# Optimization experiments

Hardware: AMD Instinct MI355X
Metric: run time of the kernel (lower is better)

Reference implementation:

```python
import jax, jax.numpy as jnp
import numpy as np

B, S, EMBED, HEADS = 2, 2048, 2048, 16
HEAD_DIM = EMBED // HEADS  # 128


def setup_inputs() -> dict:
    key = jax.random.key(0)
    k1, k2, k3 = jax.random.split(key, 3)
    x = jax.random.normal(k1, (B, S, EMBED), dtype=jnp.float32)
    # qkv_proj: Linear(EMBED -> 3*EMBED, bias=False); stored as [in, out]
    w_qkv = jax.random.normal(k2, (EMBED, 3 * EMBED), dtype=jnp.float32) / np.float32(np.sqrt(EMBED))
    # out_proj: Linear(EMBED -> EMBED, bias=False)
    w_out = jax.random.normal(k3, (EMBED, EMBED), dtype=jnp.float32) / np.float32(np.sqrt(EMBED))
    return {"x": x, "w_qkv": w_qkv, "w_out": w_out}


def reference(x, w_qkv, w_out):
    b, s, e = x.shape
    h, d = HEADS, e // HEADS
    qkv = x @ w_qkv                                  # [b, s, 3e]
    q, k, v = jnp.split(qkv, 3, axis=-1)             # each [b, s, e]
    q = q.reshape(b, s, h, d).transpose(0, 2, 1, 3)  # [b, h, s, d]
    k = k.reshape(b, s, h, d).transpose(0, 2, 1, 3)
    v = v.reshape(b, s, h, d).transpose(0, 2, 1, 3)
    scale = jnp.asarray(1.0 / np.sqrt(d), dtype=q.dtype)
    scores = jnp.einsum('bhqd,bhkd->bhqk', q, k) * scale  # [b, h, s, s]
    causal = jnp.tril(jnp.ones((s, s), dtype=bool))
    scores = jnp.where(causal, scores, -jnp.inf)
    attn = jax.nn.softmax(scores, axis=-1)
    ctx = jnp.einsum('bhqk,bhkd->bhqd', attn, v)     # [b, h, s, d]
    ctx = ctx.transpose(0, 2, 1, 3).reshape(b, s, e)
    return ctx @ w_out
```

## Files before the change

### kernel.cpp

```cpp
#include <hip/hip_runtime.h>
#include <cstdint>

#define S_LEN 2048
#define EMB   2048
#define NHEAD 16
#define HDIM  128
#define MROWS 4096
#define NQKV  6144

typedef __bf16 bf16x8 __attribute__((ext_vector_type(8)));
typedef __bf16 bf16x4 __attribute__((ext_vector_type(4)));
typedef float  f32x4  __attribute__((ext_vector_type(4)));

#define MFMA16(a, b, c) __builtin_amdgcn_mfma_f32_16x16x32_bf16((a), (b), (c), 0, 0, 0)

__device__ __forceinline__ unsigned short f2bf(float f) {
  unsigned u = __builtin_bit_cast(unsigned, f);
  u += 0x7fffu + ((u >> 16) & 1u);
  return (unsigned short)(u >> 16);
}
__device__ __forceinline__ float bf2f(unsigned short u) {
  unsigned v = ((unsigned)u) << 16;
  return __builtin_bit_cast(float, v);
}

__device__ __forceinline__ void gl_lds16(const unsigned short* g, unsigned short* l) {
  __builtin_amdgcn_global_load_lds(
      (const __attribute__((address_space(1))) void*)(uintptr_t)g,
      (__attribute__((address_space(3))) void*)(unsigned int)(uintptr_t)l,
      16, 0, 0);
}

__global__ void cast_bf16(const float* __restrict__ in, unsigned short* __restrict__ out, int n) {
  int i = (blockIdx.x * 256 + threadIdx.x) * 4;
  if (i >= n) return;
  float4 v = *(const float4*)(in + i);
  ushort4 o;
  o.x = f2bf(v.x); o.y = f2bf(v.y); o.z = f2bf(v.z); o.w = f2bf(v.w);
  *(ushort4*)(out + i) = o;
}

__global__ void transpose_cast(const float* __restrict__ in, unsigned short* __restrict__ out,
                               int R, int C) {
  __shared__ float tile[32][33];
  int bx = blockIdx.x << 5;
  int by = blockIdx.y << 5;
  int tx = threadIdx.x, ty = threadIdx.y;
  for (int j = 0; j < 32; j += 8)
    tile[ty + j][tx] = in[(size_t)(by + ty + j) * C + bx + tx];
  __syncthreads();
  for (int j = 0; j < 32; j += 8)
    out[(size_t)(bx + ty + j) * R + by + tx] = f2bf(tile[tx][ty + j]);
}

__global__ __launch_bounds__(256, 3) void gemm_qkv(const unsigned short* __restrict__ A,
                                                   const unsigned short* __restrict__ Bt,
                                                   unsigned short* __restrict__ Qo,
                                                   unsigned short* __restrict__ Ko,
                                                   unsigned short* __restrict__ Vt) {
  __shared__ __align__(16) unsigned short As[128 * 64];
  __shared__ __align__(16) unsigned short Bs[128 * 64];
  const int tid = threadIdx.x;
  const int n0 = blockIdx.x << 7;
  const int m0 = blockIdx.y << 7;
  const int wave = tid >> 6, lane = tid & 63;
  const int wm = (wave & 1) << 6, wn = (wave >> 1) << 6;
  const int fr = lane & 15, g = lane >> 4;
  const int q = tid >> 3;
  const int jp = tid & 7;
  f32x4 acc[4][4] = {};
  for (int k0 = 0; k0 < 2048; k0 += 64) {
    for (int i = 0; i < 4; ++i) {
      const int row = q + (i << 5);
      const int jsw = (jp ^ (row & 7)) << 3;
      gl_lds16(A + (size_t)(m0 + row) * 2048 + k0 + jsw, As + (row << 6) + (jp << 3));
      gl_lds16(Bt + (size_t)(n0 + row) * 2048 + k0 + jsw, Bs + (row << 6) + (jp << 3));
    }
    __builtin_amdgcn_s_waitcnt(0);
    __syncthreads();
    for (int ks = 0; ks < 2; ++ks) {
      const int slot = (((ks << 2) + g) ^ (fr & 7)) << 3;
      bf16x8 af[4], bfv[4];
      for (int i = 0; i < 4; ++i) af[i]  = *(const bf16x8*)(As + ((wm + (i << 4) + fr) << 6) + slot);
      for (int j = 0; j < 4; ++j) bfv[j] = *(const bf16x8*)(Bs + ((wn + (j << 4) + fr) << 6) + slot);
      for (int i = 0; i < 4; ++i)
        for (int j = 0; j < 4; ++j)
          acc[i][j] = MFMA16(af[i], bfv[j], acc[i][j]);
    }
    __syncthreads();
  }
  const int which = n0 >> 11;
  const int h = (n0 >> 7) & 15;
  const int bb = m0 >> 11;
  const int bh = bb * NHEAD + h;
  for (int i = 0; i < 4; ++i) {
    const int sl = (m0 & (S_LEN - 1)) + wm + (i << 4) + (g << 2);
    for (int j = 0; j < 4; ++j) {
      const int d = wn + (j << 4) + fr;
      if (which == 2) {
        ushort4 pk;
        pk.x = f2bf(acc[i][j][0]); pk.y = f2bf(acc[i][j][1]);
        pk.z = f2bf(acc[i][j][2]); pk.w = f2bf(acc[i][j][3]);
        *(ushort4*)(Vt + ((size_t)bh * HDIM + d) * S_LEN + sl) = pk;
      } else {
        unsigned short* dst = (which == 0) ? Qo : Ko;
        for (int r = 0; r < 4; ++r)
          dst[((size_t)bh * S_LEN + sl + r) * HDIM + d] = f2bf(acc[i][j][r]);
      }
    }
  }
}

__global__ __launch_bounds__(256, 3) void attn(const unsigned short* __restrict__ Qg,
                                               const unsigned short* __restrict__ Kg,
                                               const unsigned short* __restrict__ Vtg,
                                               unsigned short* __restrict__ ctx,
                                               unsigned short* __restrict__ Opart,
                                               float* __restrict__ Lp) {
  __shared__ __align__(16) unsigned short SA[16384];
  __shared__ __align__(16) unsigned short Ps[8192];
  unsigned short* Qs = SA;
  unsigned short* Ks = SA;
  unsigned short* Vs = SA + 8192;

  const int blk = blockIdx.x;
  const int bh = blk & 31;
  const int t = blk >> 5;
  int qt, kt0, nkt, part;
  if (t < 8)       { qt = t;     kt0 = 0;  nkt = 2 * t + 2;       part = -1; }
  else if (t < 16) { qt = t;     kt0 = 0;  nkt = 16;              part = (bh << 3) + (qt - 8); }
  else             { qt = t - 8; kt0 = 16; nkt = 2 * qt - 14;     part = 256 + (bh << 3) + (qt - 8); }

  const int tid = threadIdx.x, wave = tid >> 6, lane = tid & 63;
  const int fr = lane & 15, g = lane >> 4;

  const unsigned short* qsrc = Qg + ((size_t)bh * S_LEN + (qt << 7)) * HDIM;
  for (int i = 0; i < 8; ++i) {
    int s0 = (i * 256 + tid) << 3;
    int q = s0 >> 7, jp = (s0 >> 3) & 15;
    gl_lds16(qsrc + (q << 7) + ((jp ^ (q & 15)) << 3), Qs + s0);
  }
  __builtin_amdgcn_s_waitcnt(0);
  __syncthreads();

  bf16x8 qf[2][4];
  for (int nbq = 0; nbq < 2; ++nbq)
    for (int kd = 0; kd < 4; ++kd) {
      int q = (wave << 5) + (nbq << 4) + fr;
      qf[nbq][kd] = *(const bf16x8*)(Qs + (q << 7) + ((((kd << 2) + g) ^ fr) << 3));
    }
  __syncthreads();

  float lsum[2] = {0.f, 0.f};
  f32x4 oacc[2][8] = {};
  const float scale = 0.08838834764831845f;

  const unsigned short* kbase = Kg + (size_t)bh * S_LEN * HDIM;
  const unsigned short* vbase = Vtg + (size_t)bh * HDIM * S_LEN;

  for (int kti = 0; kti < nkt; ++kti) {
    const int kt = kt0 + kti;
    const unsigned short* ks = kbase + ((size_t)kt << 6) * HDIM;
    const unsigned short* vs = vbase + (kt << 6);
    for (int i = 0; i < 4; ++i) {
      int s0 = (i * 256 + tid) << 3;
      int key = s0 >> 7, jk = (s0 >> 3) & 15;
      gl_lds16(ks + (key << 7) + ((jk ^ (key & 15)) << 3), Ks + s0);
      int d = s0 >> 6, jv = (s0 >> 3) & 7;
      gl_lds16(vs + (size_t)d * S_LEN + ((jv ^ (d & 7)) << 3), Vs + s0);
    }
    __builtin_amdgcn_s_waitcnt(0);
    __syncthreads();

    f32x4 sacc[2][4] = {};
    for (int kd = 0; kd < 4; ++kd)
      for (int kb = 0; kb < 4; ++kb) {
        bf16x8 kf = *(const bf16x8*)(Ks + (((kb << 4) + fr) << 7) + ((((kd << 2) + g) ^ fr) << 3));
        sacc[0][kb] = MFMA16(kf, qf[0][kd], sacc[0][kb]);
        sacc[1][kb] = MFMA16(kf, qf[1][kd], sacc[1][kb]);
      }

    const bool diag = (kt >= 2 * qt);
    for (int nbq = 0; nbq < 2; ++nbq) {
      const int qg = (qt << 7) + (wave << 5) + (nbq << 4) + fr;
      float sum = 0.f;
      for (int kb = 0; kb < 4; ++kb) {
        float p[4];
        for (int r = 0; r < 4; ++r) {
          float v = sacc[nbq][kb][r] * scale;
          if (diag) {
            int keyg = (kt << 6) + (kb << 4) + (g << 2) + r;
            if (keyg > qg) v = -__builtin_inff();
          }
          p[r] = __expf(v);
          sum += p[r];
        }
        ushort4 pk;
        pk.x = f2bf(p[0]); pk.y = f2bf(p[1]); pk.z = f2bf(p[2]); pk.w = f2bf(p[3]);
        *(ushort4*)(Ps + (((wave << 3) + (nbq << 2) + kb) << 8) + (lane << 2)) = pk;
      }
      lsum[nbq] += sum;
    }

    __builtin_amdgcn_s_waitcnt(0);

    for (int kc = 0; kc < 2; ++kc) {
      const int kbr = (kc << 1) + (g >> 1);
      bf16x8 ap[2];
      for (int h2 = 0; h2 < 2; ++h2) {
        const unsigned short* pb =
            Ps + (((wave << 3) + (h2 << 2) + kbr) << 8) + ((g & 1) << 7) + (fr << 2);
        bf16x4 a0 = *(const bf16x4*)pb;
        bf16x4 a1 = *(const bf16x4*)(pb + 64);
        bf16x8 a;
        a[0] = a0[0]; a[1] = a0[1]; a[2] = a0[2]; a[3] = a0[3];
        a[4] = a1[0]; a[5] = a1[1]; a[6] = a1[2]; a[7] = a1[3];
        ap[h2] = a;
      }
      for (int nd = 0; nd < 8; ++nd) {
        bf16x8 bv = *(const bf16x8*)(Vs + (((nd << 4) + fr) << 6) + ((((kc << 2) + g) ^ (fr & 7)) << 3));
        oacc[0][nd] = MFMA16(ap[0], bv, oacc[0][nd]);
        oacc[1][nd] = MFMA16(ap[1], bv, oacc[1][nd]);
      }
    }
    __syncthreads();
  }

  for (int nbq = 0; nbq < 2; ++nbq) {
    lsum[nbq] += __shfl_xor(lsum[nbq], 16);
    lsum[nbq] += __shfl_xor(lsum[nbq], 32);
  }

  if (part < 0) {
    const int b = bh >> 4, h = bh & 15;
    for (int mq = 0; mq < 2; ++mq)
      for (int r = 0; r < 4; ++r) {
        float lv = __shfl(lsum[mq], (lane & 48) | ((g << 2) + r));
        const float il = 1.0f / lv;
        const int s = (qt << 7) + (wave << 5) + (mq << 4) + (g << 2) + r;
        unsigned short* dst = ctx + ((size_t)(b * S_LEN + s) * EMB) + (h << 7);
        for (int nd = 0; nd < 8; ++nd)
          dst[(nd << 4) + fr] = f2bf(oacc[mq][nd][r] * il);
      }
  } else {
    unsigned short* Ob = Opart + ((size_t)part << 14);
    for (int mq = 0; mq < 2; ++mq)
      for (int r = 0; r < 4; ++r) {
        const int ql = (wave << 5) + (mq << 4) + (g << 2) + r;
        unsigned short* dst = Ob + (ql << 7);
        for (int nd = 0; nd < 8; ++nd)
          dst[(nd << 4) + fr] = f2bf(oacc[mq][nd][r]);
      }
    if (g == 0)
      for (int nbq = 0; nbq < 2; ++nbq) {
        const int ql = (wave << 5) + (nbq << 4) + fr;
        Lp[(part << 7) + ql] = lsum[nbq];
      }
  }
}

__global__ void attn_combine(const unsigned short* __restrict__ Op,
                             const float* __restrict__ Lp,
                             unsigned short* __restrict__ ctx) {
  const int tid = threadIdx.x;
  const int rid = blockIdx.x * 16 + (tid >> 4);
  const int l16 = tid & 15;
  const int bh = rid >> 10;
  const int qtl = (rid >> 7) & 7;
  const int ql = rid & 127;
  const int p = (bh << 3) + qtl;
  const float lA = Lp[(p << 7) + ql];
  const float lB = Lp[((256 + p) << 7) + ql];
  const float il = 1.0f / (lA + lB);
  const int d0 = l16 << 3;
  const unsigned short* a = Op + ((size_t)p << 14) + (ql << 7) + d0;
  const unsigned short* b = Op + ((size_t)(256 + p) << 14) + (ql << 7) + d0;
  const int bb = bh >> 4, h = bh & 15;
  const int s = ((qtl + 8) << 7) + ql;
  unsigned short* dst = ctx + ((size_t)(bb * S_LEN + s) * EMB) + (h << 7) + d0;
  ushort4 va0 = *(const ushort4*)a, va1 = *(const ushort4*)(a + 4);
  ushort4 vb0 = *(const ushort4*)b, vb1 = *(const ushort4*)(b + 4);
  ushort4 o0, o1;
  o0.x = f2bf((bf2f(va0.x) + bf2f(vb0.x)) * il);
  o0.y = f2bf((bf2f(va0.y) + bf2f(vb0.y)) * il);
  o0.z = f2bf((bf2f(va0.z) + bf2f(vb0.z)) * il);
  o0.w = f2bf((bf2f(va0.w) + bf2f(vb0.w)) * il);
  o1.x = f2bf((bf2f(va1.x) + bf2f(vb1.x)) * il);
  o1.y = f2bf((bf2f(va1.y) + bf2f(vb1.y)) * il);
  o1.z = f2bf((bf2f(va1.z) + bf2f(vb1.z)) * il);
  o1.w = f2bf((bf2f(va1.w) + bf2f(vb1.w)) * il);
  *(ushort4*)dst = o0;
  *(ushort4*)(dst + 4) = o1;
}

__global__ __launch_bounds__(256, 3) void gemm_out(const unsigned short* __restrict__ A,
                                                   const unsigned short* __restrict__ Bt,
                                                   float* __restrict__ C) {
  __shared__ __align__(16) unsigned short As[128 * 64];
  __shared__ __align__(16) unsigned short Bs[128 * 64];
  const int tid = threadIdx.x;
  const int n0 = blockIdx.x << 7;
  const int m0 = blockIdx.y << 7;
  const int wave = tid >> 6, lane = tid & 63;
  const int wm = (wave & 1) << 6, wn = (wave >> 1) << 6;
  const int fr = lane & 15, g = lane >> 4;
  const int q = tid >> 3;
  const int jp = tid & 7;
  f32x4 acc[4][4] = {};
  for (int k0 = 0; k0 < 2048; k0 += 64) {
    for (int i = 0; i < 4; ++i) {
      const int row = q + (i << 5);
      const int jsw = (jp ^ (row & 7)) << 3;
      gl_lds16(A + (size_t)(m0 + row) * 2048 + k0 + jsw, As + (row << 6) + (jp << 3));
      gl_lds16(Bt + (size_t)(n0 + row) * 2048 + k0 + jsw, Bs + (row << 6) + (jp << 3));
    }
    __builtin_amdgcn_s_waitcnt(0);
    __syncthreads();
    for (int ks = 0; ks < 2; ++ks) {
      const int slot = (((ks << 2) + g) ^ (fr & 7)) << 3;
      bf16x8 af[4], bfv[4];
      for (int i = 0; i < 4; ++i) af[i]  = *(const bf16x8*)(As + ((wm + (i << 4) + fr) << 6) + slot);
      for (int j = 0; j < 4; ++j) bfv[j] = *(const bf16x8*)(Bs + ((wn + (j << 4) + fr) << 6) + slot);
      for (int i = 0; i < 4; ++i)
        for (int j = 0; j < 4; ++j)
          acc[i][j] = MFMA16(af[i], bfv[j], acc[i][j]);
    }
    __syncthreads();
  }
  for (int i = 0; i < 4; ++i) {
    const int row = m0 + wm + (i << 4) + (g << 2);
    for (int j = 0; j < 4; ++j) {
      const int col = n0 + wn + (j << 4) + fr;
      for (int r = 0; r < 4; ++r)
        C[(size_t)(row + r) * EMB + col] = acc[i][j][r];
    }
  }
}

extern "C" void kernel_launch(void* const* d_in, const int* in_sizes, int n_in,
                              void* d_out, int out_size, void* d_ws, size_t ws_size,
                              hipStream_t stream) {
  const float* x    = (const float*)d_in[0];
  const float* wqkv = (const float*)d_in[1];
  const float* wout = (const float*)d_in[2];
  float* out = (float*)d_out;

  unsigned short* ws = (unsigned short*)d_ws;
  const size_t NELEM = (size_t)MROWS * EMB;
  unsigned short* xb    = ws;
  unsigned short* wqkvT = xb + NELEM;
  unsigned short* woutT = wqkvT + (size_t)NQKV * EMB;
  unsigned short* Q     = woutT + (size_t)EMB * EMB;
  unsigned short* K     = Q + NELEM;
  unsigned short* Vt    = K + NELEM;
  unsigned short* ctx   = xb;
  unsigned short* Opart = wqkvT;
  float* Lp = (float*)(Opart + ((size_t)512 << 14));

  cast_bf16<<<8192, 256, 0, stream>>>(x, xb, (int)NELEM);
  transpose_cast<<<dim3(NQKV / 32, EMB / 32), dim3(32, 8), 0, stream>>>(wqkv, wqkvT, EMB, NQKV);
  transpose_cast<<<dim3(EMB / 32, EMB / 32), dim3(32, 8), 0, stream>>>(wout, woutT, EMB, EMB);
  gemm_qkv<<<dim3(NQKV / 128, MROWS / 128), 256, 0, stream>>>(xb, wqkvT, Q, K, Vt);
  attn<<<768, 256, 0, stream>>>(Q, K, Vt, ctx, Opart, Lp);
  attn_combine<<<2048, 256, 0, stream>>>(Opart, Lp, ctx);
  gemm_out<<<dim3(EMB / 128, MROWS / 128), 256, 0, stream>>>(ctx, woutT, out);
}
```

Baseline: 380.4 us.

## Rebalance causal attention splits, shrink P buffer, vectorize weight transpose

Query tiles are now split into 1, 2 or 3 key-range chunks depending on causal length, giving 960 blocks of more even work instead of a fixed two-way split. The combine kernel is generalised to sum a variable number of partials. The score/softmax/PV loop is reworked to handle 32 keys at a time, which halves the P staging buffer so four blocks can fit per CU, and it uses exp2 with a pre-multiplied log2e scale. The weight transpose-cast now uses 64x64 tiles with float4 loads and ushort4 stores. The finer split adds more partial-output traffic and combine work in exchange for better load balance and occupancy.

```diff
diff --git a/kernel.cpp b/kernel.cpp
--- a/kernel.cpp
+++ b/kernel.cpp
@@ -42,15 +42,25 @@
 
 __global__ void transpose_cast(const float* __restrict__ in, unsigned short* __restrict__ out,
                                int R, int C) {
-  __shared__ float tile[32][33];
-  int bx = blockIdx.x << 5;
-  int by = blockIdx.y << 5;
-  int tx = threadIdx.x, ty = threadIdx.y;
-  for (int j = 0; j < 32; j += 8)
-    tile[ty + j][tx] = in[(size_t)(by + ty + j) * C + bx + tx];
+  __shared__ float tile[64][65];
+  const int bx = blockIdx.x << 6;
+  const int by = blockIdx.y << 6;
+  const int tid = threadIdx.x;
+  const int ty = tid >> 4, cx = (tid & 15) << 2;
+  for (int i = 0; i < 4; ++i) {
+    const int r = ty + (i << 4);
+    float4 v = *(const float4*)(in + (size_t)(by + r) * C + bx + cx);
+    tile[r][cx] = v.x; tile[r][cx + 1] = v.y; tile[r][cx + 2] = v.z; tile[r][cx + 3] = v.w;
+  }
   __syncthreads();
-  for (int j = 0; j < 32; j += 8)
-    out[(size_t)(bx + ty + j) * R + by + tx] = f2bf(tile[tx][ty + j]);
+  const int r4 = (tid & 15) << 2, c0 = tid >> 4;
+  for (int m = 0; m < 4; ++m) {
+    const int c = c0 + (m << 4);
+    ushort4 o;
+    o.x = f2bf(tile[r4][c]);     o.y = f2bf(tile[r4 + 1][c]);
+    o.z = f2bf(tile[r4 + 2][c]); o.w = f2bf(tile[r4 + 3][c]);
+    *(ushort4*)(out + (size_t)(bx + c) * R + by + r4) = o;
+  }
 }
 
 __global__ __launch_bounds__(256, 3) void gemm_qkv(const unsigned short* __restrict__ A,
@@ -111,14 +121,14 @@
   }
 }
 
-__global__ __launch_bounds__(256, 3) void attn(const unsigned short* __restrict__ Qg,
+__global__ __launch_bounds__(256, 4) void attn(const unsigned short* __restrict__ Qg,
                                                const unsigned short* __restrict__ Kg,
                                                const unsigned short* __restrict__ Vtg,
                                                unsigned short* __restrict__ ctx,
                                                unsigned short* __restrict__ Opart,
                                                float* __restrict__ Lp) {
   __shared__ __align__(16) unsigned short SA[16384];
-  __shared__ __align__(16) unsigned short Ps[8192];
+  __shared__ __align__(16) unsigned short Ps[4096];
   unsigned short* Qs = SA;
   unsigned short* Ks = SA;
   unsigned short* Vs = SA + 8192;
@@ -126,19 +136,33 @@
   const int blk = blockIdx.x;
   const int bh = blk & 31;
   const int t = blk >> 5;
-  int qt, kt0, nkt, part;
-  if (t < 8)       { qt = t;     kt0 = 0;  nkt = 2 * t + 2;       part = -1; }
-  else if (t < 16) { qt = t;     kt0 = 0;  nkt = 16;              part = (bh << 3) + (qt - 8); }
-  else             { qt = t - 8; kt0 = 16; nkt = 2 * qt - 14;     part = 256 + (bh << 3) + (qt - 8); }
+  int qt, kt0, nkt, slot;
+  if (t < 6) {
+    qt = t; kt0 = 0; nkt = 2 * t + 2; slot = -1;
+  } else if (t < 18) {
+    const int i = t - 6, c = i & 1;
+    qt = 6 + (i >> 1);
+    const int h = qt + 1;
+    kt0 = c * h; nkt = h;
+    slot = bh * 24 + ((qt - 6) << 1) + c;
+  } else {
+    const int i = t - 18, q3 = i / 3, c = i - 3 * q3;
+    qt = 12 + q3;
+    const int T = 2 * qt + 2;
+    const int s0 = (T + 2) / 3, s1 = (T + 1) / 3;
+    kt0 = (c == 0) ? 0 : ((c == 1) ? s0 : (s0 + s1));
+    nkt = (c == 0) ? s0 : ((c == 1) ? s1 : (T - s0 - s1));
+    slot = bh * 24 + 12 + q3 * 3 + c;
+  }
 
   const int tid = threadIdx.x, wave = tid >> 6, lane = tid & 63;
   const int fr = lane & 15, g = lane >> 4;
 
   const unsigned short* qsrc = Qg + ((size_t)bh * S_LEN + (qt << 7)) * HDIM;
   for (int i = 0; i < 8; ++i) {
-    int s0 = (i * 256 + tid) << 3;
-    int q = s0 >> 7, jp = (s0 >> 3) & 15;
-    gl_lds16(qsrc + (q << 7) + ((jp ^ (q & 15)) << 3), Qs + s0);
+    int s0q = (i * 256 + tid) << 3;
+    int q = s0q >> 7, jp = (s0q >> 3) & 15;
+    gl_lds16(qsrc + (q << 7) + ((jp ^ (q & 15)) << 3), Qs + s0q);
   }
   __builtin_amdgcn_s_waitcnt(0);
   __syncthreads();
@@ -153,7 +177,7 @@
 
   float lsum[2] = {0.f, 0.f};
   f32x4 oacc[2][8] = {};
-  const float scale = 0.08838834764831845f;
+  const float scale2 = 0.12751672753f;
 
   const unsigned short* kbase = Kg + (size_t)bh * S_LEN * HDIM;
   const unsigned short* vbase = Vtg + (size_t)bh * HDIM * S_LEN;
@@ -163,53 +187,52 @@
     const unsigned short* ks = kbase + ((size_t)kt << 6) * HDIM;
     const unsigned short* vs = vbase + (kt << 6);
     for (int i = 0; i < 4; ++i) {
-      int s0 = (i * 256 + tid) << 3;
-      int key = s0 >> 7, jk = (s0 >> 3) & 15;
-      gl_lds16(ks + (key << 7) + ((jk ^ (key & 15)) << 3), Ks + s0);
-      int d = s0 >> 6, jv = (s0 >> 3) & 7;
-      gl_lds16(vs + (size_t)d * S_LEN + ((jv ^ (d & 7)) << 3), Vs + s0);
+      int s0s = (i * 256 + tid) << 3;
+      int key = s0s >> 7, jk = (s0s >> 3) & 15;
+      gl_lds16(ks + (key << 7) + ((jk ^ (key & 15)) << 3), Ks + s0s);
+      int d = s0s >> 6, jv = (s0s >> 3) & 7;
+      gl_lds16(vs + (size_t)d * S_LEN + ((jv ^ (d & 7)) << 3), Vs + s0s);
     }
     __builtin_amdgcn_s_waitcnt(0);
     __syncthreads();
 
-    f32x4 sacc[2][4] = {};
-    for (int kd = 0; kd < 4; ++kd)
-      for (int kb = 0; kb < 4; ++kb) {
-        bf16x8 kf = *(const bf16x8*)(Ks + (((kb << 4) + fr) << 7) + ((((kd << 2) + g) ^ fr) << 3));
-        sacc[0][kb] = MFMA16(kf, qf[0][kd], sacc[0][kb]);
-        sacc[1][kb] = MFMA16(kf, qf[1][kd], sacc[1][kb]);
-      }
-
     const bool diag = (kt >= 2 * qt);
-    for (int nbq = 0; nbq < 2; ++nbq) {
-      const int qg = (qt << 7) + (wave << 5) + (nbq << 4) + fr;
-      float sum = 0.f;
-      for (int kb = 0; kb < 4; ++kb) {
-        float p[4];
-        for (int r = 0; r < 4; ++r) {
-          float v = sacc[nbq][kb][r] * scale;
-          if (diag) {
-            int keyg = (kt << 6) + (kb << 4) + (g << 2) + r;
-            if (keyg > qg) v = -__builtin_inff();
+    for (int kc = 0; kc < 2; ++kc) {
+      f32x4 sacc[2][2] = {};
+      for (int kd = 0; kd < 4; ++kd)
+        for (int kb2 = 0; kb2 < 2; ++kb2) {
+          const int kb = (kc << 1) | kb2;
+          bf16x8 kf = *(const bf16x8*)(Ks + (((kb << 4) + fr) << 7) + ((((kd << 2) + g) ^ fr) << 3));
+          sacc[0][kb2] = MFMA16(kf, qf[0][kd], sacc[0][kb2]);
+          sacc[1][kb2] = MFMA16(kf, qf[1][kd], sacc[1][kb2]);
+        }
+
+      for (int nbq = 0; nbq < 2; ++nbq) {
+        const int qg = (qt << 7) + (wave << 5) + (nbq << 4) + fr;
+        float sum = 0.f;
+        for (int kb2 = 0; kb2 < 2; ++kb2) {
+          const int kb = (kc << 1) | kb2;
+          float p[4];
+          for (int r = 0; r < 4; ++r) {
+            float v = sacc[nbq][kb2][r] * scale2;
+            if (diag) {
+              int keyg = (kt << 6) + (kb << 4) + (g << 2) + r;
+              if (keyg > qg) v = -__builtin_inff();
+            }
+            p[r] = exp2f(v);
+            sum += p[r];
           }
-          p[r] = __expf(v);
-          sum += p[r];
+          ushort4 pk;
+          pk.x = f2bf(p[0]); pk.y = f2bf(p[1]); pk.z = f2bf(p[2]); pk.w = f2bf(p[3]);
+          *(ushort4*)(Ps + (((wave << 2) | (nbq << 1) | kb2) << 8) + (lane << 2)) = pk;
         }
-        ushort4 pk;
-        pk.x = f2bf(p[0]); pk.y = f2bf(p[1]); pk.z = f2bf(p[2]); pk.w = f2bf(p[3]);
-        *(ushort4*)(Ps + (((wave << 3) + (nbq << 2) + kb) << 8) + (lane << 2)) = pk;
-      }
-      lsum[nbq] += sum;
-    }
-
-    __builtin_amdgcn_s_waitcnt(0);
-
-    for (int kc = 0; kc < 2; ++kc) {
-      const int kbr = (kc << 1) + (g >> 1);
+        lsum[nbq] += sum;
+      }
+
       bf16x8 ap[2];
       for (int h2 = 0; h2 < 2; ++h2) {
         const unsigned short* pb =
-            Ps + (((wave << 3) + (h2 << 2) + kbr) << 8) + ((g & 1) << 7) + (fr << 2);
+            Ps + (((wave << 2) | (h2 << 1) | (g >> 1)) << 8) + ((g & 1) << 7) + (fr << 2);
         bf16x4 a0 = *(const bf16x4*)pb;
         bf16x4 a1 = *(const bf16x4*)(pb + 64);
         bf16x8 a;
@@ -231,7 +254,7 @@
     lsum[nbq] += __shfl_xor(lsum[nbq], 32);
   }
 
-  if (part < 0) {
+  if (slot < 0) {
     const int b = bh >> 4, h = bh & 15;
     for (int mq = 0; mq < 2; ++mq)
       for (int r = 0; r < 4; ++r) {
@@ -243,7 +266,7 @@
           dst[(nd << 4) + fr] = f2bf(oacc[mq][nd][r] * il);
       }
   } else {
-    unsigned short* Ob = Opart + ((size_t)part << 14);
+    unsigned short* Ob = Opart + ((size_t)slot << 14);
     for (int mq = 0; mq < 2; ++mq)
       for (int r = 0; r < 4; ++r) {
         const int ql = (wave << 5) + (mq << 4) + (g << 2) + r;
@@ -254,7 +277,7 @@
     if (g == 0)
       for (int nbq = 0; nbq < 2; ++nbq) {
         const int ql = (wave << 5) + (nbq << 4) + fr;
-        Lp[(part << 7) + ql] = lsum[nbq];
+        Lp[(slot << 7) + ql] = lsum[nbq];
       }
   }
 }
@@ -264,31 +287,30 @@
                              unsigned short* __restrict__ ctx) {
   const int tid = threadIdx.x;
   const int rid = blockIdx.x * 16 + (tid >> 4);
-  const int l16 = tid & 15;
-  const int bh = rid >> 10;
-  const int qtl = (rid >> 7) & 7;
+  const int qtIdx = rid >> 12;
+  const int bh = (rid >> 7) & 31;
   const int ql = rid & 127;
-  const int p = (bh << 3) + qtl;
-  const float lA = Lp[(p << 7) + ql];
-  const float lB = Lp[((256 + p) << 7) + ql];
-  const float il = 1.0f / (lA + lB);
-  const int d0 = l16 << 3;
-  const unsigned short* a = Op + ((size_t)p << 14) + (ql << 7) + d0;
-  const unsigned short* b = Op + ((size_t)(256 + p) << 14) + (ql << 7) + d0;
+  const int qt = 6 + qtIdx;
+  const int nc = (qt < 12) ? 2 : 3;
+  const int sb = bh * 24 + ((qt < 12) ? ((qt - 6) << 1) : (12 + (qt - 12) * 3));
+  const int d0 = (tid & 15) << 3;
+  float l = 0.f;
+  float o[8] = {};
+  for (int c = 0; c < nc; ++c) {
+    const int slot = sb + c;
+    l += Lp[(slot << 7) + ql];
+    const unsigned short* a = Op + ((size_t)slot << 14) + (ql << 7) + d0;
+    ushort4 v0 = *(const ushort4*)a, v1 = *(const ushort4*)(a + 4);
+    o[0] += bf2f(v0.x); o[1] += bf2f(v0.y); o[2] += bf2f(v0.z); o[3] += bf2f(v0.w);
+    o[4] += bf2f(v1.x); o[5] += bf2f(v1.y); o[6] += bf2f(v1.z); o[7] += bf2f(v1.w);
+  }
+  const float il = 1.0f / l;
   const int bb = bh >> 4, h = bh & 15;
-  const int s = ((qtl + 8) << 7) + ql;
+  const int s = (qt << 7) + ql;
   unsigned short* dst = ctx + ((size_t)(bb * S_LEN + s) * EMB) + (h << 7) + d0;
-  ushort4 va0 = *(const ushort4*)a, va1 = *(const ushort4*)(a + 4);
-  ushort4 vb0 = *(const ushort4*)b, vb1 = *(const ushort4*)(b + 4);
   ushort4 o0, o1;
-  o0.x = f2bf((bf2f(va0.x) + bf2f(vb0.x)) * il);
-  o0.y = f2bf((bf2f(va0.y) + bf2f(vb0.y)) * il);
-  o0.z = f2bf((bf2f(va0.z) + bf2f(vb0.z)) * il);
-  o0.w = f2bf((bf2f(va0.w) + bf2f(vb0.w)) * il);
-  o1.x = f2bf((bf2f(va1.x) + bf2f(vb1.x)) * il);
-  o1.y = f2bf((bf2f(va1.y) + bf2f(vb1.y)) * il);
-  o1.z = f2bf((bf2f(va1.z) + bf2f(vb1.z)) * il);
-  o1.w = f2bf((bf2f(va1.w) + bf2f(vb1.w)) * il);
+  o0.x = f2bf(o[0] * il); o0.y = f2bf(o[1] * il); o0.z = f2bf(o[2] * il); o0.w = f2bf(o[3] * il);
+  o1.x = f2bf(o[4] * il); o1.y = f2bf(o[5] * il); o1.z = f2bf(o[6] * il); o1.w = f2bf(o[7] * il);
   *(ushort4*)dst = o0;
   *(ushort4*)(dst + 4) = o1;
 }
@@ -355,13 +377,13 @@
   unsigned short* Vt    = K + NELEM;
   unsigned short* ctx   = xb;
   unsigned short* Opart = wqkvT;
-  float* Lp = (float*)(Opart + ((size_t)512 << 14));
+  float* Lp = (float*)(Vt + NELEM);
 
   cast_bf16<<<8192, 256, 0, stream>>>(x, xb, (int)NELEM);
-  transpose_cast<<<dim3(NQKV / 32, EMB / 32), dim3(32, 8), 0, stream>>>(wqkv, wqkvT, EMB, NQKV);
-  transpose_cast<<<dim3(EMB / 32, EMB / 32), dim3(32, 8), 0, stream>>>(wout, woutT, EMB, EMB);
+  transpose_cast<<<dim3(NQKV / 64, EMB / 64), 256, 0, stream>>>(wqkv, wqkvT, EMB, NQKV);
+  transpose_cast<<<dim3(EMB / 64, EMB / 64), 256, 0, stream>>>(wout, woutT, EMB, EMB);
   gemm_qkv<<<dim3(NQKV / 128, MROWS / 128), 256, 0, stream>>>(xb, wqkvT, Q, K, Vt);
-  attn<<<768, 256, 0, stream>>>(Q, K, Vt, ctx, Opart, Lp);
-  attn_combine<<<2048, 256, 0, stream>>>(Opart, Lp, ctx);
+  attn<<<960, 256, 0, stream>>>(Q, K, Vt, ctx, Opart, Lp);
+  attn_combine<<<2560, 256, 0, stream>>>(Opart, Lp, ctx);
   gemm_out<<<dim3(EMB / 128, MROWS / 128), 256, 0, stream>>>(ctx, woutT, out);
 }
```

Result: slower. 525.3 us (+38.1%).
